# Kernel optimization log

Hardware: AMD Instinct MI355X
Metric: run time of the kernel (lower is better)

The kernel has to match this reference:

```python
import jax, jax.numpy as jnp
import numpy as np

HIDDEN = 2048
NUM_HEADS = 16
HEAD_DIM = 128
WINDOW = 1024
ROPE_THETA = 10000.0
B, L = 1, 4096


def setup_inputs() -> dict:
    key = jax.random.key(0)
    k0, k1, k2, k3, k4 = jax.random.split(key, 5)
    s = 1.0 / np.sqrt(HIDDEN)
    return {
        "hidden_states": jax.random.normal(k0, (B, L, HIDDEN), dtype=jnp.float32),
        "wq": jax.random.normal(k1, (HIDDEN, NUM_HEADS * HEAD_DIM), dtype=jnp.float32) * s,
        "wk": jax.random.normal(k2, (HIDDEN, NUM_HEADS * HEAD_DIM), dtype=jnp.float32) * s,
        "wv": jax.random.normal(k3, (HIDDEN, NUM_HEADS * HEAD_DIM), dtype=jnp.float32) * s,
        "wo": jax.random.normal(k4, (NUM_HEADS * HEAD_DIM, HIDDEN), dtype=jnp.float32) * s,
    }


def _apply_rotary(x, cos, sin):
    # x: [B, H, L, D]; cos/sin: [L, D/2]
    d2 = x.shape[-1] // 2
    x1, x2 = x[..., :d2], x[..., d2:]
    return jnp.concatenate([x1 * cos - x2 * sin, x2 * cos + x1 * sin], axis=-1)


def reference(hidden_states, wq, wk, wv, wo):
    Bsz, Ln, _ = hidden_states.shape
    dtype = hidden_states.dtype
    scale = HEAD_DIM ** (-0.5)

    def split_heads(x):
        return x.reshape(Bsz, Ln, NUM_HEADS, HEAD_DIM).transpose(0, 2, 1, 3)

    q = split_heads(hidden_states @ wq)
    k = split_heads(hidden_states @ wk)
    v = split_heads(hidden_states @ wv)

    inv_freq = 1.0 / (ROPE_THETA ** (jnp.arange(0, HEAD_DIM, 2, dtype=jnp.float32) / HEAD_DIM))
    pos = jnp.arange(Ln, dtype=jnp.float32)
    freqs = pos[:, None] * inv_freq[None, :]  # [L, D/2]
    cos = jnp.cos(freqs).astype(dtype)
    sin = jnp.sin(freqs).astype(dtype)

    q = _apply_rotary(q, cos, sin)
    k = _apply_rotary(k, cos, sin)

    q_pos = jnp.arange(Ln)[:, None]
    k_pos = jnp.arange(Ln)[None, :]
    valid = (k_pos > q_pos - WINDOW) & (k_pos <= q_pos)  # [L, L]
    neg = jnp.finfo(dtype).min

    attn = jnp.einsum("bhqd,bhkd->bhqk", q, k) * scale
    attn = jnp.where(valid, attn, neg)
    attn = jax.nn.softmax(attn, axis=-1)
    out = jnp.einsum("bhqk,bhkd->bhqd", attn, v)
    out = out.transpose(0, 2, 1, 3).reshape(Bsz, Ln, NUM_HEADS * HEAD_DIM)
    return out @ wo
```

## Files before the change

kernel.cpp:

```cpp
#include <hip/hip_runtime.h>
#include <cstdint>
#include <cstddef>

typedef unsigned short u16;
typedef __bf16 bf16x8 __attribute__((ext_vector_type(8)));
typedef float f32x4 __attribute__((ext_vector_type(4)));
typedef unsigned short u16x8 __attribute__((ext_vector_type(8)));

#define SEQ 4096
#define HID 2048
#define NH 16
#define HD 128
#define WIN 1024

__device__ __forceinline__ float bf2f(u16 u) {
  union { unsigned int i; float f; } v; v.i = ((unsigned int)u) << 16; return v.f;
}
__device__ __forceinline__ u16 f2bf(float f) {
  union { float f; unsigned int i; } v; v.f = f;
  unsigned int r = v.i + 0x7FFFu + ((v.i >> 16) & 1u);
  return (u16)(r >> 16);
}
__device__ __forceinline__ u16 f2bf_rne(float f) {
  union { __bf16 b; u16 u; } v; v.b = (__bf16)f; return v.u;
}
__device__ __forceinline__ float exp2a(float x) {
  float r; asm("v_exp_f32 %0, %1" : "=v"(r) : "v"(x)); return r;
}
template<int L2R>
__device__ __forceinline__ unsigned swz(unsigned o) { return o ^ (((o >> L2R) & 7u) << 4); }

__device__ __forceinline__ void gload_lds16(const u16* g, u16* l) {
  __builtin_amdgcn_global_load_lds((const __attribute__((address_space(1))) void*)g,
                                   (__attribute__((address_space(3))) void*)l, 16, 0, 0);
}


__global__ void cast_f32_bf16(const float* __restrict__ in, u16* __restrict__ out, int n4) {
  int i = blockIdx.x * blockDim.x + threadIdx.x;
  if (i < n4) {
    float4 v = ((const float4*)in)[i];
    union { u16 u[4]; unsigned long long ll; } r;
    r.u[0] = f2bf(v.x); r.u[1] = f2bf(v.y); r.u[2] = f2bf(v.z); r.u[3] = f2bf(v.w);
    ((unsigned long long*)out)[i] = r.ll;
  }
}

__global__ void transpose_cast4(const float* __restrict__ w0, const float* __restrict__ w1,
                                const float* __restrict__ w2, const float* __restrict__ w3,
                                u16* __restrict__ o0, u16* __restrict__ o1,
                                u16* __restrict__ o2, u16* __restrict__ o3) {
  __shared__ float t[32][33];
  const float* W = (blockIdx.z == 0) ? w0 : (blockIdx.z == 1) ? w1 : (blockIdx.z == 2) ? w2 : w3;
  u16* Wt = (blockIdx.z == 0) ? o0 : (blockIdx.z == 1) ? o1 : (blockIdx.z == 2) ? o2 : o3;
  const int tx = threadIdx.x & 31, ty = threadIdx.x >> 5;
  const int x0 = blockIdx.x * 32, y0 = blockIdx.y * 32;
#pragma unroll
  for (int i = 0; i < 4; ++i)
    t[ty + i * 8][tx] = W[(size_t)(y0 + ty + i * 8) * HID + x0 + tx];
  __syncthreads();
#pragma unroll
  for (int i = 0; i < 4; ++i)
    Wt[(size_t)(x0 + ty + i * 8) * HID + y0 + tx] = f2bf(t[tx][ty + i * 8]);
}

__global__ void rope_table(float* __restrict__ ctab, float* __restrict__ stab) {
  int idx = blockIdx.x * blockDim.x + threadIdx.x;
  int pos = idx >> 6, i = idx & 63;
  float invf = expf(-(float)i * 0.14391156831212787f);
  float ang = (float)pos * invf;
  float s, c;
  sincosf(ang, &s, &c);
  ctab[idx] = c; stab[idx] = s;
}

__global__ void rope_apply(u16* __restrict__ Qb, u16* __restrict__ Kb,
                           const float* __restrict__ ctab, const float* __restrict__ stab) {
  int idx = blockIdx.x * blockDim.x + threadIdx.x;
  int pos = idx >> 10;
  int rem = idx & 1023;
  int h = rem >> 6, i = rem & 63;
  size_t base = (size_t)pos * HID + h * HD + i;
  float c = ctab[(pos << 6) + i], s = stab[(pos << 6) + i];
  float q1 = bf2f(Qb[base]), q2 = bf2f(Qb[base + 64]);
  Qb[base] = f2bf(q1 * c - q2 * s);
  Qb[base + 64] = f2bf(q2 * c + q1 * s);
  float k1 = bf2f(Kb[base]), k2 = bf2f(Kb[base + 64]);
  Kb[base] = f2bf(k1 * c - k2 * s);
  Kb[base + 64] = f2bf(k2 * c + k1 * s);
}


template<bool OUT_F32>
__device__ __forceinline__ void gemm_body(const u16* __restrict__ A, const u16* __restrict__ Bt,
                                          void* __restrict__ C, int brow, int bcol,
                                          u16 (&ldsA)[2][8192], u16 (&ldsB)[2][8192]) {
  const int lane = threadIdx.x & 63;
  const int wv = threadIdx.x >> 6;
  const int wr = wv >> 1, wc = wv & 1;
  const int K = HID, N = HID;

  const f32x4 zero = {0.f, 0.f, 0.f, 0.f};
  f32x4 acc[4][4];
#pragma unroll
  for (int m = 0; m < 4; ++m)
#pragma unroll
    for (int n = 0; n < 4; ++n) acc[m][n] = zero;

  auto stage = [&](int buf, int kt) {
    const int k0 = kt * 64;
#pragma unroll
    for (int i = 0; i < 4; ++i) {
      unsigned o = ((unsigned)(wv * 4 + i) * 64 + (unsigned)lane) * 16u;
      unsigned r = o >> 7;
      unsigned cb = swz<7>(o) & 127u;
      const size_t gcol = (size_t)k0 + (cb >> 1);
      gload_lds16(A + (size_t)(brow + r) * K + gcol, &ldsA[buf][(wv * 4 + i) * 512]);
      gload_lds16(Bt + (size_t)(bcol + r) * K + gcol, &ldsB[buf][(wv * 4 + i) * 512]);
    }
  };

  stage(0, 0);
  __syncthreads();
  int buf = 0;
  const int nt = K / 64;
  for (int kt = 0; kt < nt; ++kt) {
    if (kt + 1 < nt) stage(buf ^ 1, kt + 1);
    __builtin_amdgcn_s_setprio(1);
#pragma unroll
    for (int s = 0; s < 2; ++s) {
      const unsigned kb = (unsigned)(s * 64 + ((lane >> 4) & 3) * 16);
      bf16x8 af[4], bfv[4];
#pragma unroll
      for (int m = 0; m < 4; ++m) {
        unsigned row = wr * 64 + m * 16 + (lane & 15);
        af[m] = *(const bf16x8*)((const char*)&ldsA[buf][0] + swz<7>(row * 128 + kb));
      }
#pragma unroll
      for (int n = 0; n < 4; ++n) {
        unsigned row = wc * 64 + n * 16 + (lane & 15);
        bfv[n] = *(const bf16x8*)((const char*)&ldsB[buf][0] + swz<7>(row * 128 + kb));
      }
#pragma unroll
      for (int m = 0; m < 4; ++m)
#pragma unroll
        for (int n = 0; n < 4; ++n)
          acc[m][n] = __builtin_amdgcn_mfma_f32_16x16x32_bf16(af[m], bfv[n], acc[m][n], 0, 0, 0);
    }
    __builtin_amdgcn_s_setprio(0);
    __syncthreads();
    buf ^= 1;
  }

#pragma unroll
  for (int m = 0; m < 4; ++m) {
    const int rbase = brow + wr * 64 + m * 16 + ((lane >> 4) & 3) * 4;
#pragma unroll
    for (int n = 0; n < 4; ++n) {
      const int cbase = bcol + wc * 64 + n * 16 + (lane & 15);
#pragma unroll
      for (int r = 0; r < 4; ++r) {
        const size_t idx = (size_t)(rbase + r) * N + cbase;
        if (OUT_F32) ((float*)C)[idx] = acc[m][n][r];
        else ((u16*)C)[idx] = f2bf(acc[m][n][r]);
      }
    }
  }
}

__global__ __launch_bounds__(256, 2) void gemm_qkv_kernel(
    const u16* __restrict__ X, const u16* __restrict__ Wqt, const u16* __restrict__ Wkt,
    const u16* __restrict__ Wvt, u16* __restrict__ Qo, u16* __restrict__ Ko, u16* __restrict__ Vo) {
  __shared__ u16 ldsA[2][8192];
  __shared__ u16 ldsB[2][8192];
  int flat = (blockIdx.z * 32 + blockIdx.y) * 16 + blockIdx.x;
  int nf = (flat & 7) * 192 + (flat >> 3);
  int bx = nf & 15, by = (nf >> 4) & 31, bz = nf >> 9;
  const u16* Bt = (bz == 0) ? Wqt : (bz == 1) ? Wkt : Wvt;
  u16* C = (bz == 0) ? Qo : (bz == 1) ? Ko : Vo;
  gemm_body<false>(X, Bt, C, by * 128, bx * 128, ldsA, ldsB);
}

__global__ __launch_bounds__(256, 2) void gemm_out_kernel(
    const u16* __restrict__ Ob, const u16* __restrict__ Wot, float* __restrict__ out) {
  __shared__ u16 ldsA[2][8192];
  __shared__ u16 ldsB[2][8192];
  int flat = blockIdx.y * 16 + blockIdx.x;
  int nf = (flat & 7) * 64 + (flat >> 3);
  int bx = nf & 15, by = nf >> 4;
  gemm_body<true>(Ob, Wot, out, by * 128, bx * 128, ldsA, ldsB);
}


__global__ __launch_bounds__(256, 2) void attn_kernel(
    const u16* __restrict__ Q, const u16* __restrict__ K,
    const u16* __restrict__ V, u16* __restrict__ O) {
  __shared__ u16 k_lds[2][8192];
  __shared__ u16 vt_lds[2][8192];
  __shared__ u16 p_lds[4][1024];

  const int lane = threadIdx.x & 63;
  const int wv = threadIdx.x >> 6;
  const int g = lane >> 4;
  const int c = lane & 15;

  int flat = blockIdx.y * 64 + blockIdx.x;
  int nf = (flat & 7) * 128 + (flat >> 3);
  const int q0 = (nf & 63) * 64;
  const int h = nf >> 6;

#pragma unroll
  for (int i = 0; i < 4; ++i) {
    unsigned o = ((unsigned)(wv * 4 + i) * 64 + (unsigned)lane) * 16u;
    unsigned r = o >> 8;
    unsigned cb = swz<8>(o) & 255u;
    gload_lds16(Q + (size_t)(q0 + r) * HID + h * HD + (cb >> 1), &k_lds[0][(wv * 4 + i) * 512]);
  }
  __syncthreads();
  bf16x8 qf[4];
#pragma unroll
  for (int s = 0; s < 4; ++s) {
    unsigned row = wv * 16 + c;
    qf[s] = *(const bf16x8*)((const char*)&k_lds[0][0] + swz<8>(row * 256 + s * 64 + g * 16));
  }
  __syncthreads();

  const int t_start = (q0 >= WIN) ? (q0 - WIN) : 0;

#pragma unroll
  for (int i = 0; i < 4; ++i) {
    unsigned o = ((unsigned)(wv * 4 + i) * 64 + (unsigned)lane) * 16u;
    unsigned r = o >> 8;
    unsigned cb = swz<8>(o) & 255u;
    gload_lds16(K + (size_t)(t_start + r) * HID + h * HD + (cb >> 1), &k_lds[0][(wv * 4 + i) * 512]);
  }
  {
    const u16x8* src = (const u16x8*)(V + (size_t)(t_start + lane) * HID + h * HD + wv * 32);
#pragma unroll
    for (int it = 0; it < 4; ++it) {
      u16x8 vv = src[it];
#pragma unroll
      for (int j = 0; j < 8; ++j) {
        const int d = wv * 32 + it * 8 + j;
        vt_lds[0][d * 64 + (lane ^ ((d & 7) << 3))] = vv[j];
      }
    }
  }
  __syncthreads();

  const f32x4 zero = {0.f, 0.f, 0.f, 0.f};
  float mrow[4], lrow[4];
  f32x4 oacc[8];
#pragma unroll
  for (int r = 0; r < 4; ++r) { mrow[r] = -1e30f; lrow[r] = 0.f; }
#pragma unroll
  for (int d = 0; d < 8; ++d) oacc[d] = zero;

  const float scale2 = 0.12751743f;
  int b = 0;

  for (int t0 = t_start; t0 <= q0; t0 += 64) {
    const int nb = b ^ 1;
    const bool has_next = (t0 + 64 <= q0);

    u16x8 vr[4];
    if (has_next) {
#pragma unroll
      for (int i = 0; i < 4; ++i) {
        unsigned o = ((unsigned)(wv * 4 + i) * 64 + (unsigned)lane) * 16u;
        unsigned r = o >> 8;
        unsigned cb = swz<8>(o) & 255u;
        gload_lds16(K + (size_t)(t0 + 64 + r) * HID + h * HD + (cb >> 1),
                    &k_lds[nb][(wv * 4 + i) * 512]);
      }
      const u16x8* src = (const u16x8*)(V + (size_t)(t0 + 64 + lane) * HID + h * HD + wv * 32);
#pragma unroll
      for (int it = 0; it < 4; ++it) vr[it] = src[it];
    }

    f32x4 sa[4];
#pragma unroll
    for (int kf = 0; kf < 4; ++kf) sa[kf] = zero;
    __builtin_amdgcn_s_setprio(1);
#pragma unroll
    for (int s = 0; s < 4; ++s) {
#pragma unroll
      for (int kf = 0; kf < 4; ++kf) {
        unsigned row = kf * 16 + c;
        bf16x8 kb = *(const bf16x8*)((const char*)&k_lds[b][0] + swz<8>(row * 256 + s * 64 + g * 16));
        sa[kf] = __builtin_amdgcn_mfma_f32_16x16x32_bf16(qf[s], kb, sa[kf], 0, 0, 0);
      }
    }
    __builtin_amdgcn_s_setprio(0);

    const int qbase = q0 + wv * 16 + g * 4;
    const bool diag = (t0 == q0);
    const bool lowm = (q0 >= WIN) && (t0 == t_start);
    if (diag) {
#pragma unroll
      for (int kf = 0; kf < 4; ++kf) {
        const int kpos = t0 + kf * 16 + c;
#pragma unroll
        for (int r = 0; r < 4; ++r) {
          float x = sa[kf][r] * scale2;
          sa[kf][r] = (kpos <= qbase + r) ? x : -1e30f;
        }
      }
    } else if (lowm) {
#pragma unroll
      for (int kf = 0; kf < 4; ++kf) {
        const int kpos = t0 + kf * 16 + c;
#pragma unroll
        for (int r = 0; r < 4; ++r) {
          float x = sa[kf][r] * scale2;
          sa[kf][r] = (kpos > qbase + r - WIN) ? x : -1e30f;
        }
      }
    } else {
#pragma unroll
      for (int kf = 0; kf < 4; ++kf)
#pragma unroll
        for (int r = 0; r < 4; ++r) sa[kf][r] *= scale2;
    }

    float tmax[4];
#pragma unroll
    for (int r = 0; r < 4; ++r)
      tmax[r] = fmaxf(fmaxf(sa[0][r], sa[1][r]), fmaxf(sa[2][r], sa[3][r]));
#pragma unroll
    for (int r = 0; r < 4; ++r)
#pragma unroll
      for (int d = 1; d < 16; d <<= 1)
        tmax[r] = fmaxf(tmax[r], __shfl_xor(tmax[r], d, 16));

    bool okl = (tmax[0] <= mrow[0] + 8.f) && (tmax[1] <= mrow[1] + 8.f) &&
               (tmax[2] <= mrow[2] + 8.f) && (tmax[3] <= mrow[3] + 8.f);
    if (!__all((int)okl)) {
#pragma unroll
      for (int r = 0; r < 4; ++r) {
        const float mn = fmaxf(mrow[r], tmax[r]);
        const float al = exp2a(mrow[r] - mn);
        mrow[r] = mn;
        lrow[r] *= al;
#pragma unroll
        for (int df = 0; df < 8; ++df) oacc[df][r] *= al;
      }
    }

    float rs[4] = {0.f, 0.f, 0.f, 0.f};
    if (diag || lowm) {
#pragma unroll
      for (int kf = 0; kf < 4; ++kf)
#pragma unroll
        for (int r = 0; r < 4; ++r) {
          const float x = sa[kf][r];
          const float p = (x < -1e29f) ? 0.f : exp2a(x - mrow[r]);
          sa[kf][r] = p; rs[r] += p;
        }
    } else {
#pragma unroll
      for (int kf = 0; kf < 4; ++kf)
#pragma unroll
        for (int r = 0; r < 4; ++r) {
          const float p = exp2a(sa[kf][r] - mrow[r]);
          sa[kf][r] = p; rs[r] += p;
        }
    }
#pragma unroll
    for (int r = 0; r < 4; ++r) {
#pragma unroll
      for (int d = 1; d < 16; d <<= 1) rs[r] += __shfl_xor(rs[r], d, 16);
      lrow[r] += rs[r];
    }

#pragma unroll
    for (int kf = 0; kf < 4; ++kf)
#pragma unroll
      for (int r = 0; r < 4; ++r) {
        const int q = g * 4 + r;
        p_lds[wv][q * 64 + ((kf * 16 + c) ^ ((q & 7) << 3))] = f2bf_rne(sa[kf][r]);
      }

    if (has_next) {
#pragma unroll
      for (int it = 0; it < 4; ++it)
#pragma unroll
        for (int j = 0; j < 8; ++j) {
          const int d = wv * 32 + it * 8 + j;
          vt_lds[nb][d * 64 + (lane ^ ((d & 7) << 3))] = vr[it][j];
        }
    }

    asm volatile("" ::: "memory");

    __builtin_amdgcn_s_setprio(1);
#pragma unroll
    for (int s2 = 0; s2 < 2; ++s2) {
      const bf16x8 pa = *(const bf16x8*)&p_lds[wv][c * 64 + ((s2 * 32 + g * 8) ^ ((c & 7) << 3))];
#pragma unroll
      for (int df = 0; df < 8; ++df) {
        const int row = df * 16 + c;
        const bf16x8 vb = *(const bf16x8*)&vt_lds[b][row * 64 + ((s2 * 32 + g * 8) ^ ((row & 7) << 3))];
        oacc[df] = __builtin_amdgcn_mfma_f32_16x16x32_bf16(pa, vb, oacc[df], 0, 0, 0);
      }
    }
    __builtin_amdgcn_s_setprio(0);
    __syncthreads();
    b = nb;
  }

  float invl[4];
#pragma unroll
  for (int r = 0; r < 4; ++r) invl[r] = 1.f / lrow[r];
#pragma unroll
  for (int df = 0; df < 8; ++df)
#pragma unroll
    for (int r = 0; r < 4; ++r) {
      const int row = q0 + wv * 16 + g * 4 + r;
      const int col = h * HD + df * 16 + c;
      O[(size_t)row * HID + col] = f2bf(oacc[df][r] * invl[r]);
    }
}


extern "C" void kernel_launch(void* const* d_in, const int* in_sizes, int n_in,
                              void* d_out, int out_size, void* d_ws, size_t ws_size,
                              hipStream_t stream) {
  const float* hidden = (const float*)d_in[0];
  const float* wq = (const float*)d_in[1];
  const float* wk = (const float*)d_in[2];
  const float* wv = (const float*)d_in[3];
  const float* wo = (const float*)d_in[4];
  float* out = (float*)d_out;

  char* ws = (char*)d_ws;
  u16* Xb  = (u16*)ws;                 ws += (size_t)SEQ * HID * 2;
  u16* Wqt = (u16*)ws;                 ws += (size_t)HID * HID * 2;
  u16* Wkt = (u16*)ws;                 ws += (size_t)HID * HID * 2;
  u16* Wvt = (u16*)ws;                 ws += (size_t)HID * HID * 2;
  u16* Wot = (u16*)ws;                 ws += (size_t)HID * HID * 2;
  u16* Qb  = (u16*)ws;                 ws += (size_t)SEQ * HID * 2;
  u16* Kb  = (u16*)ws;                 ws += (size_t)SEQ * HID * 2;
  u16* Vb  = (u16*)ws;                 ws += (size_t)SEQ * HID * 2;
  u16* Ob  = (u16*)ws;                 ws += (size_t)SEQ * HID * 2;
  float* ctab = (float*)ws;            ws += (size_t)SEQ * 64 * 4;
  float* stab = (float*)ws;            ws += (size_t)SEQ * 64 * 4;

  cast_f32_bf16<<<(SEQ * HID / 4 + 255) / 256, 256, 0, stream>>>(hidden, Xb, SEQ * HID / 4);

  dim3 tg(64, 64, 4);
  transpose_cast4<<<tg, 256, 0, stream>>>(wq, wk, wv, wo, Wqt, Wkt, Wvt, Wot);

  rope_table<<<(SEQ * 64) / 256, 256, 0, stream>>>(ctab, stab);

  dim3 gq(HID / 128, SEQ / 128, 3);
  gemm_qkv_kernel<<<gq, 256, 0, stream>>>(Xb, Wqt, Wkt, Wvt, Qb, Kb, Vb);

  rope_apply<<<(SEQ * NH * 64) / 256, 256, 0, stream>>>(Qb, Kb, ctab, stab);

  dim3 ga(SEQ / 64, NH);
  attn_kernel<<<ga, 256, 0, stream>>>(Qb, Kb, Vb, Ob);

  dim3 go(HID / 128, SEQ / 128);
  gemm_out_kernel<<<go, 256, 0, stream>>>(Ob, Wot, out);
}
```

Before: 291.4 us.

## Use 256x128 eight-wave GEMM tiles with triple-buffered LDS and explicit vmcnt waits

Both the QKV and output projection GEMMs move from 128x128 tiles on 4 waves to 256x128 tiles on 8 waves. The K-loop now prefetches two stages ahead into three LDS buffers and uses explicit s_waitcnt vmcnt thresholds plus raw barriers instead of __syncthreads. The goal is to hide global-load latency better and raise arithmetic intensity per B-tile load. In exchange, each block needs about 144KB of LDS, so only one block fits per CU despite the launch bounds, and the halved grid gives coarser load balance.

Measured after the change: 317.3 us. 1.09x slower.

```diff
diff --git a/kernel.cpp b/kernel.cpp
--- a/kernel.cpp
+++ b/kernel.cpp
@@ -92,12 +92,14 @@
 
 
 template<bool OUT_F32>
-__device__ __forceinline__ void gemm_body(const u16* __restrict__ A, const u16* __restrict__ Bt,
-                                          void* __restrict__ C, int brow, int bcol,
-                                          u16 (&ldsA)[2][8192], u16 (&ldsB)[2][8192]) {
+__device__ __forceinline__ void gemm8_body(const u16* __restrict__ A, const u16* __restrict__ Bt,
+                                           void* __restrict__ C, int brow, int bcol,
+                                           u16 (&ldsA)[3][16384], u16 (&ldsB)[3][8192]) {
   const int lane = threadIdx.x & 63;
   const int wv = threadIdx.x >> 6;
   const int wr = wv >> 1, wc = wv & 1;
+  const int g = lane >> 4, c = lane & 15;
+  const int tid = threadIdx.x;
   const int K = HID, N = HID;
 
   const f32x4 zero = {0.f, 0.f, 0.f, 0.f};
@@ -111,53 +113,76 @@
     const int k0 = kt * 64;
 #pragma unroll
     for (int i = 0; i < 4; ++i) {
-      unsigned o = ((unsigned)(wv * 4 + i) * 64 + (unsigned)lane) * 16u;
+      unsigned idx = (unsigned)(i * 512 + tid);
+      unsigned o = idx * 16u;
       unsigned r = o >> 7;
       unsigned cb = swz<7>(o) & 127u;
-      const size_t gcol = (size_t)k0 + (cb >> 1);
-      gload_lds16(A + (size_t)(brow + r) * K + gcol, &ldsA[buf][(wv * 4 + i) * 512]);
-      gload_lds16(Bt + (size_t)(bcol + r) * K + gcol, &ldsB[buf][(wv * 4 + i) * 512]);
+      gload_lds16(A + (size_t)(brow + r) * K + k0 + (cb >> 1), &ldsA[buf][idx * 8]);
+    }
+#pragma unroll
+    for (int i = 0; i < 2; ++i) {
+      unsigned idx = (unsigned)(i * 512 + tid);
+      unsigned o = idx * 16u;
+      unsigned r = o >> 7;
+      unsigned cb = swz<7>(o) & 127u;
+      gload_lds16(Bt + (size_t)(bcol + r) * K + k0 + (cb >> 1), &ldsB[buf][idx * 8]);
     }
   };
 
+  const int nt = K / 64;
   stage(0, 0);
-  __syncthreads();
-  int buf = 0;
-  const int nt = K / 64;
+  stage(1, 1);
+
+  int bc = 0, bs = 2;
   for (int kt = 0; kt < nt; ++kt) {
-    if (kt + 1 < nt) stage(buf ^ 1, kt + 1);
+    if (kt + 2 < nt) {
+      stage(bs, kt + 2);
+      asm volatile("s_waitcnt vmcnt(12)" ::: "memory");
+    } else if (kt + 1 < nt) {
+      asm volatile("s_waitcnt vmcnt(6)" ::: "memory");
+    } else {
+      asm volatile("s_waitcnt vmcnt(0)" ::: "memory");
+    }
+    __builtin_amdgcn_s_barrier();
+    asm volatile("" ::: "memory");
+
+    bf16x8 af[4][2], bfv[4][2];
+#pragma unroll
+    for (int m = 0; m < 4; ++m) {
+      const unsigned row = (unsigned)(wr * 64 + m * 16 + c);
+#pragma unroll
+      for (int ks = 0; ks < 2; ++ks)
+        af[m][ks] = *(const bf16x8*)((const char*)&ldsA[bc][0] + swz<7>(row * 128 + ks * 64 + g * 16));
+    }
+#pragma unroll
+    for (int n = 0; n < 4; ++n) {
+      const unsigned row = (unsigned)(wc * 64 + n * 16 + c);
+#pragma unroll
+      for (int ks = 0; ks < 2; ++ks)
+        bfv[n][ks] = *(const bf16x8*)((const char*)&ldsB[bc][0] + swz<7>(row * 128 + ks * 64 + g * 16));
+    }
     __builtin_amdgcn_s_setprio(1);
 #pragma unroll
-    for (int s = 0; s < 2; ++s) {
-      const unsigned kb = (unsigned)(s * 64 + ((lane >> 4) & 3) * 16);
-      bf16x8 af[4], bfv[4];
-#pragma unroll
-      for (int m = 0; m < 4; ++m) {
-        unsigned row = wr * 64 + m * 16 + (lane & 15);
-        af[m] = *(const bf16x8*)((const char*)&ldsA[buf][0] + swz<7>(row * 128 + kb));
-      }
-#pragma unroll
-      for (int n = 0; n < 4; ++n) {
-        unsigned row = wc * 64 + n * 16 + (lane & 15);
-        bfv[n] = *(const bf16x8*)((const char*)&ldsB[buf][0] + swz<7>(row * 128 + kb));
-      }
+    for (int ks = 0; ks < 2; ++ks)
 #pragma unroll
       for (int m = 0; m < 4; ++m)
 #pragma unroll
         for (int n = 0; n < 4; ++n)
-          acc[m][n] = __builtin_amdgcn_mfma_f32_16x16x32_bf16(af[m], bfv[n], acc[m][n], 0, 0, 0);
-    }
+          acc[m][n] = __builtin_amdgcn_mfma_f32_16x16x32_bf16(af[m][ks], bfv[n][ks], acc[m][n], 0, 0, 0);
     __builtin_amdgcn_s_setprio(0);
-    __syncthreads();
-    buf ^= 1;
+
+    asm volatile("s_waitcnt lgkmcnt(0)" ::: "memory");
+    __builtin_amdgcn_s_barrier();
+    bc = (bc == 2) ? 0 : bc + 1;
+    bs = (bs == 2) ? 0 : bs + 1;
   }
 
 #pragma unroll
   for (int m = 0; m < 4; ++m) {
-    const int rbase = brow + wr * 64 + m * 16 + ((lane >> 4) & 3) * 4;
+    const int rbase = brow + wr * 64 + m * 16 + g * 4;
 #pragma unroll
     for (int n = 0; n < 4; ++n) {
-      const int cbase = bcol + wc * 64 + n * 16 + (lane & 15);
+      const int cbase = bcol + wc * 64 + n * 16 + c;
 #pragma unroll
       for (int r = 0; r < 4; ++r) {
         const size_t idx = (size_t)(rbase + r) * N + cbase;
@@ -168,27 +193,27 @@
   }
 }
 
-__global__ __launch_bounds__(256, 2) void gemm_qkv_kernel(
+__global__ __launch_bounds__(512, 2) void gemm_qkv_kernel(
     const u16* __restrict__ X, const u16* __restrict__ Wqt, const u16* __restrict__ Wkt,
     const u16* __restrict__ Wvt, u16* __restrict__ Qo, u16* __restrict__ Ko, u16* __restrict__ Vo) {
-  __shared__ u16 ldsA[2][8192];
-  __shared__ u16 ldsB[2][8192];
-  int flat = (blockIdx.z * 32 + blockIdx.y) * 16 + blockIdx.x;
-  int nf = (flat & 7) * 192 + (flat >> 3);
-  int bx = nf & 15, by = (nf >> 4) & 31, bz = nf >> 9;
+  __shared__ u16 ldsA[3][16384];
+  __shared__ u16 ldsB[3][8192];
+  int flat = (blockIdx.z * 16 + blockIdx.y) * 16 + blockIdx.x;
+  int nf = (flat & 7) * 96 + (flat >> 3);
+  int bx = nf & 15, by = (nf >> 4) & 15, bz = nf >> 8;
   const u16* Bt = (bz == 0) ? Wqt : (bz == 1) ? Wkt : Wvt;
-  u16* C = (bz == 0) ? Qo : (bz == 1) ? Ko : Vo;
-  gemm_body<false>(X, Bt, C, by * 128, bx * 128, ldsA, ldsB);
-}
-
-__global__ __launch_bounds__(256, 2) void gemm_out_kernel(
+  u16* Cp = (bz == 0) ? Qo : (bz == 1) ? Ko : Vo;
+  gemm8_body<false>(X, Bt, Cp, by * 256, bx * 128, ldsA, ldsB);
+}
+
+__global__ __launch_bounds__(512, 2) void gemm_out_kernel(
     const u16* __restrict__ Ob, const u16* __restrict__ Wot, float* __restrict__ out) {
-  __shared__ u16 ldsA[2][8192];
-  __shared__ u16 ldsB[2][8192];
+  __shared__ u16 ldsA[3][16384];
+  __shared__ u16 ldsB[3][8192];
   int flat = blockIdx.y * 16 + blockIdx.x;
-  int nf = (flat & 7) * 64 + (flat >> 3);
+  int nf = (flat & 7) * 32 + (flat >> 3);
   int bx = nf & 15, by = nf >> 4;
-  gemm_body<true>(Ob, Wot, out, by * 128, bx * 128, ldsA, ldsB);
+  gemm8_body<true>(Ob, Wot, out, by * 256, bx * 128, ldsA, ldsB);
 }
 
 
@@ -453,14 +478,14 @@
 
   rope_table<<<(SEQ * 64) / 256, 256, 0, stream>>>(ctab, stab);
 
-  dim3 gq(HID / 128, SEQ / 128, 3);
-  gemm_qkv_kernel<<<gq, 256, 0, stream>>>(Xb, Wqt, Wkt, Wvt, Qb, Kb, Vb);
+  dim3 gq(16, 16, 3);
+  gemm_qkv_kernel<<<gq, 512, 0, stream>>>(Xb, Wqt, Wkt, Wvt, Qb, Kb, Vb);
 
   rope_apply<<<(SEQ * NH * 64) / 256, 256, 0, stream>>>(Qb, Kb, ctab, stab);
 
   dim3 ga(SEQ / 64, NH);
   attn_kernel<<<ga, 256, 0, stream>>>(Qb, Kb, Vb, Ob);
 
-  dim3 go(HID / 128, SEQ / 128);
-  gemm_out_kernel<<<go, 256, 0, stream>>>(Ob, Wot, out);
-}
+  dim3 go(16, 16);
+  gemm_out_kernel<<<go, 512, 0, stream>>>(Ob, Wot, out);
+}
```

## Fuse rotary embedding into QKV GEMM epilogue and retile waves per head

Applied to the files above, without the earlier changes.

Removes the separate rope_apply kernel by applying the rotary rotation in the QKV GEMM epilogue on fp32 accumulators. The wave tiling changes so each wave covers 32 rows by the full 128-column head, which puts both rotary halves in the same thread. This saves a full read/write pass over Q and K plus a kernel launch. The cost is more B-fragment LDS reads per wave and extra cos/sin table loads in the epilogue.

After: 283.0 us. 2.9% less time.

```diff
diff --git a/kernel.cpp b/kernel.cpp
--- a/kernel.cpp
+++ b/kernel.cpp
@@ -74,38 +74,31 @@
   ctab[idx] = c; stab[idx] = s;
 }
 
-__global__ void rope_apply(u16* __restrict__ Qb, u16* __restrict__ Kb,
-                           const float* __restrict__ ctab, const float* __restrict__ stab) {
-  int idx = blockIdx.x * blockDim.x + threadIdx.x;
-  int pos = idx >> 10;
-  int rem = idx & 1023;
-  int h = rem >> 6, i = rem & 63;
-  size_t base = (size_t)pos * HID + h * HD + i;
-  float c = ctab[(pos << 6) + i], s = stab[(pos << 6) + i];
-  float q1 = bf2f(Qb[base]), q2 = bf2f(Qb[base + 64]);
-  Qb[base] = f2bf(q1 * c - q2 * s);
-  Qb[base + 64] = f2bf(q2 * c + q1 * s);
-  float k1 = bf2f(Kb[base]), k2 = bf2f(Kb[base + 64]);
-  Kb[base] = f2bf(k1 * c - k2 * s);
-  Kb[base + 64] = f2bf(k2 * c + k1 * s);
-}
-
-
-template<bool OUT_F32>
-__device__ __forceinline__ void gemm_body(const u16* __restrict__ A, const u16* __restrict__ Bt,
-                                          void* __restrict__ C, int brow, int bcol,
-                                          u16 (&ldsA)[2][8192], u16 (&ldsB)[2][8192]) {
+
+__global__ __launch_bounds__(256, 2) void gemm_qkv_kernel(
+    const u16* __restrict__ X, const u16* __restrict__ Wqt, const u16* __restrict__ Wkt,
+    const u16* __restrict__ Wvt, u16* __restrict__ Qo, u16* __restrict__ Ko, u16* __restrict__ Vo,
+    const float* __restrict__ ctab, const float* __restrict__ stab) {
+  __shared__ u16 ldsA[2][8192];
+  __shared__ u16 ldsB[2][8192];
+  int flat = (blockIdx.z * 32 + blockIdx.y) * 16 + blockIdx.x;
+  int nf = (flat & 7) * 192 + (flat >> 3);
+  int bx = nf & 15, by = (nf >> 4) & 31, bz = nf >> 9;
+  const u16* Bt = (bz == 0) ? Wqt : (bz == 1) ? Wkt : Wvt;
+  u16* Cp = (bz == 0) ? Qo : (bz == 1) ? Ko : Vo;
+  const int brow = by * 128, bcol = bx * 128;
+
   const int lane = threadIdx.x & 63;
   const int wv = threadIdx.x >> 6;
-  const int wr = wv >> 1, wc = wv & 1;
+  const int g = lane >> 4, c = lane & 15;
   const int K = HID, N = HID;
 
   const f32x4 zero = {0.f, 0.f, 0.f, 0.f};
-  f32x4 acc[4][4];
-#pragma unroll
-  for (int m = 0; m < 4; ++m)
-#pragma unroll
-    for (int n = 0; n < 4; ++n) acc[m][n] = zero;
+  f32x4 acc[2][8];
+#pragma unroll
+  for (int m = 0; m < 2; ++m)
+#pragma unroll
+    for (int n = 0; n < 8; ++n) acc[m][n] = zero;
 
   auto stage = [&](int buf, int kt) {
     const int k0 = kt * 64;
@@ -115,7 +108,7 @@
       unsigned r = o >> 7;
       unsigned cb = swz<7>(o) & 127u;
       const size_t gcol = (size_t)k0 + (cb >> 1);
-      gload_lds16(A + (size_t)(brow + r) * K + gcol, &ldsA[buf][(wv * 4 + i) * 512]);
+      gload_lds16(X + (size_t)(brow + r) * K + gcol, &ldsA[buf][(wv * 4 + i) * 512]);
       gload_lds16(Bt + (size_t)(bcol + r) * K + gcol, &ldsB[buf][(wv * 4 + i) * 512]);
     }
   };
@@ -129,22 +122,22 @@
     __builtin_amdgcn_s_setprio(1);
 #pragma unroll
     for (int s = 0; s < 2; ++s) {
-      const unsigned kb = (unsigned)(s * 64 + ((lane >> 4) & 3) * 16);
-      bf16x8 af[4], bfv[4];
-#pragma unroll
-      for (int m = 0; m < 4; ++m) {
-        unsigned row = wr * 64 + m * 16 + (lane & 15);
+      const unsigned kb = (unsigned)(s * 64 + g * 16);
+      bf16x8 af[2], bfv[8];
+#pragma unroll
+      for (int m = 0; m < 2; ++m) {
+        unsigned row = wv * 32 + m * 16 + c;
         af[m] = *(const bf16x8*)((const char*)&ldsA[buf][0] + swz<7>(row * 128 + kb));
       }
 #pragma unroll
-      for (int n = 0; n < 4; ++n) {
-        unsigned row = wc * 64 + n * 16 + (lane & 15);
+      for (int n = 0; n < 8; ++n) {
+        unsigned row = n * 16 + c;
         bfv[n] = *(const bf16x8*)((const char*)&ldsB[buf][0] + swz<7>(row * 128 + kb));
       }
 #pragma unroll
-      for (int m = 0; m < 4; ++m)
-#pragma unroll
-        for (int n = 0; n < 4; ++n)
+      for (int m = 0; m < 2; ++m)
+#pragma unroll
+        for (int n = 0; n < 8; ++n)
           acc[m][n] = __builtin_amdgcn_mfma_f32_16x16x32_bf16(af[m], bfv[n], acc[m][n], 0, 0, 0);
     }
     __builtin_amdgcn_s_setprio(0);
@@ -152,34 +145,41 @@
     buf ^= 1;
   }
 
-#pragma unroll
-  for (int m = 0; m < 4; ++m) {
-    const int rbase = brow + wr * 64 + m * 16 + ((lane >> 4) & 3) * 4;
-#pragma unroll
-    for (int n = 0; n < 4; ++n) {
-      const int cbase = bcol + wc * 64 + n * 16 + (lane & 15);
+  if (bz < 2) {
+#pragma unroll
+    for (int m = 0; m < 2; ++m) {
+      const int rbase = brow + wv * 32 + m * 16 + g * 4;
 #pragma unroll
       for (int r = 0; r < 4; ++r) {
-        const size_t idx = (size_t)(rbase + r) * N + cbase;
-        if (OUT_F32) ((float*)C)[idx] = acc[m][n][r];
-        else ((u16*)C)[idx] = f2bf(acc[m][n][r]);
-      }
-    }
-  }
-}
-
-__global__ __launch_bounds__(256, 2) void gemm_qkv_kernel(
-    const u16* __restrict__ X, const u16* __restrict__ Wqt, const u16* __restrict__ Wkt,
-    const u16* __restrict__ Wvt, u16* __restrict__ Qo, u16* __restrict__ Ko, u16* __restrict__ Vo) {
-  __shared__ u16 ldsA[2][8192];
-  __shared__ u16 ldsB[2][8192];
-  int flat = (blockIdx.z * 32 + blockIdx.y) * 16 + blockIdx.x;
-  int nf = (flat & 7) * 192 + (flat >> 3);
-  int bx = nf & 15, by = (nf >> 4) & 31, bz = nf >> 9;
-  const u16* Bt = (bz == 0) ? Wqt : (bz == 1) ? Wkt : Wvt;
-  u16* C = (bz == 0) ? Qo : (bz == 1) ? Ko : Vo;
-  gemm_body<false>(X, Bt, C, by * 128, bx * 128, ldsA, ldsB);
-}
+        const int pos = rbase + r;
+        const float* cp = ctab + (size_t)pos * 64;
+        const float* sp = stab + (size_t)pos * 64;
+        u16* crow = Cp + (size_t)pos * N + bcol;
+#pragma unroll
+        for (int n = 0; n < 4; ++n) {
+          const int i = n * 16 + c;
+          const float x1 = acc[m][n][r], x2 = acc[m][n + 4][r];
+          const float co = cp[i], si = sp[i];
+          crow[i] = f2bf(x1 * co - x2 * si);
+          crow[i + 64] = f2bf(x2 * co + x1 * si);
+        }
+      }
+    }
+  } else {
+#pragma unroll
+    for (int m = 0; m < 2; ++m) {
+      const int rbase = brow + wv * 32 + m * 16 + g * 4;
+#pragma unroll
+      for (int r = 0; r < 4; ++r) {
+        u16* crow = Cp + (size_t)(rbase + r) * N + bcol;
+#pragma unroll
+        for (int n = 0; n < 8; ++n)
+          crow[n * 16 + c] = f2bf(acc[m][n][r]);
+      }
+    }
+  }
+}
+
 
 __global__ __launch_bounds__(256, 2) void gemm_out_kernel(
     const u16* __restrict__ Ob, const u16* __restrict__ Wot, float* __restrict__ out) {
@@ -188,7 +188,77 @@
   int flat = blockIdx.y * 16 + blockIdx.x;
   int nf = (flat & 7) * 64 + (flat >> 3);
   int bx = nf & 15, by = nf >> 4;
-  gemm_body<true>(Ob, Wot, out, by * 128, bx * 128, ldsA, ldsB);
+  const int brow = by * 128, bcol = bx * 128;
+
+  const int lane = threadIdx.x & 63;
+  const int wv = threadIdx.x >> 6;
+  const int wr = wv >> 1, wc = wv & 1;
+  const int g = lane >> 4, c = lane & 15;
+  const int K = HID, N = HID;
+
+  const f32x4 zero = {0.f, 0.f, 0.f, 0.f};
+  f32x4 acc[4][4];
+#pragma unroll
+  for (int m = 0; m < 4; ++m)
+#pragma unroll
+    for (int n = 0; n < 4; ++n) acc[m][n] = zero;
+
+  auto stage = [&](int buf, int kt) {
+    const int k0 = kt * 64;
+#pragma unroll
+    for (int i = 0; i < 4; ++i) {
+      unsigned o = ((unsigned)(wv * 4 + i) * 64 + (unsigned)lane) * 16u;
+      unsigned r = o >> 7;
+      unsigned cb = swz<7>(o) & 127u;
+      const size_t gcol = (size_t)k0 + (cb >> 1);
+      gload_lds16(Ob + (size_t)(brow + r) * K + gcol, &ldsA[buf][(wv * 4 + i) * 512]);
+      gload_lds16(Wot + (size_t)(bcol + r) * K + gcol, &ldsB[buf][(wv * 4 + i) * 512]);
+    }
+  };
+
+  stage(0, 0);
+  __syncthreads();
+  int buf = 0;
+  const int nt = K / 64;
+  for (int kt = 0; kt < nt; ++kt) {
+    if (kt + 1 < nt) stage(buf ^ 1, kt + 1);
+    __builtin_amdgcn_s_setprio(1);
+#pragma unroll
+    for (int s = 0; s < 2; ++s) {
+      const unsigned kb = (unsigned)(s * 64 + g * 16);
+      bf16x8 af[4], bfv[4];
+#pragma unroll
+      for (int m = 0; m < 4; ++m) {
+        unsigned row = wr * 64 + m * 16 + c;
+        af[m] = *(const bf16x8*)((const char*)&ldsA[buf][0] + swz<7>(row * 128 + kb));
+      }
+#pragma unroll
+      for (int n = 0; n < 4; ++n) {
+        unsigned row = wc * 64 + n * 16 + c;
+        bfv[n] = *(const bf16x8*)((const char*)&ldsB[buf][0] + swz<7>(row * 128 + kb));
+      }
+#pragma unroll
+      for (int m = 0; m < 4; ++m)
+#pragma unroll
+        for (int n = 0; n < 4; ++n)
+          acc[m][n] = __builtin_amdgcn_mfma_f32_16x16x32_bf16(af[m], bfv[n], acc[m][n], 0, 0, 0);
+    }
+    __builtin_amdgcn_s_setprio(0);
+    __syncthreads();
+    buf ^= 1;
+  }
+
+#pragma unroll
+  for (int m = 0; m < 4; ++m) {
+    const int rbase = brow + wr * 64 + m * 16 + g * 4;
+#pragma unroll
+    for (int n = 0; n < 4; ++n) {
+      const int cbase = bcol + wc * 64 + n * 16 + c;
+#pragma unroll
+      for (int r = 0; r < 4; ++r)
+        out[(size_t)(rbase + r) * N + cbase] = acc[m][n][r];
+    }
+  }
 }
 
 
@@ -454,9 +524,7 @@
   rope_table<<<(SEQ * 64) / 256, 256, 0, stream>>>(ctab, stab);
 
   dim3 gq(HID / 128, SEQ / 128, 3);
-  gemm_qkv_kernel<<<gq, 256, 0, stream>>>(Xb, Wqt, Wkt, Wvt, Qb, Kb, Vb);
-
-  rope_apply<<<(SEQ * NH * 64) / 256, 256, 0, stream>>>(Qb, Kb, ctab, stab);
+  gemm_qkv_kernel<<<gq, 256, 0, stream>>>(Xb, Wqt, Wkt, Wvt, Qb, Kb, Vb, ctab, stab);
 
   dim3 ga(SEQ / 64, NH);
   attn_kernel<<<ga, 256, 0, stream>>>(Qb, Kb, Vb, Ob);
```
